# Optimization experiments

Measured on AMD Instinct MI355X. Metric: run time of the kernel, lower is better.

Reference implementation:

```python
import jax, jax.numpy as jnp
import numpy as np

B, N, E = 8, 2048, 2048  # requires N == E (see bmm(value, attn^T) constraint)

def setup_inputs() -> dict:
    key = jax.random.key(0)
    k1, k2, k3 = jax.random.split(key, 3)
    inputs = jax.random.normal(k1, (B, N, E), dtype=jnp.float32)
    # nn.Linear(embed_size, embed_size): weight [E,E], bias [E]
    W = jax.random.normal(k2, (E, E), dtype=jnp.float32) * (1.0 / np.sqrt(E))
    b = jax.random.normal(k3, (E,), dtype=jnp.float32) * 0.01
    gamma = jnp.zeros((), dtype=jnp.float32)  # nn.Parameter(torch.tensor(0.0))
    return {"inputs": inputs, "W": W, "b": b, "gamma": gamma}

def reference(inputs, W, b, gamma):
    # query = Linear(inputs); key = value = inputs
    query = jnp.einsum('bne,fe->bnf', inputs, W) + b          # [B,N,E]
    # scores = bmm(query, key^T) + gamma  -> [B,N,N]
    scores = jnp.einsum('bne,bme->bnm', query, inputs) + gamma
    # softmax over dim=1 (rows, NOT the usual last dim)
    attn = jax.nn.softmax(scores, axis=1)                      # [B,N,N]
    # output = bmm(value, attn^T): out[b,n,m] = sum_e value[b,n,e]*attn[b,m,e]
    out = jnp.einsum('bne,bme->bnm', inputs, attn)             # [B,N,N]
    return out
```

## Files before the change

### kernel.cpp

```cpp
#include <hip/hip_runtime.h>
#include <stdint.h>


typedef _Float16 f16;
typedef f16 f16x8 __attribute__((ext_vector_type(8)));
typedef f16 f16x4 __attribute__((ext_vector_type(4)));
typedef float f32x4 __attribute__((ext_vector_type(4)));

#define ND 2048
#define NNL 4194304L
#define NT 32

static __device__ __forceinline__ void stage16(const void* g, void* l) {
  __builtin_amdgcn_global_load_lds(
      (const __attribute__((address_space(1))) uint32_t*)g,
      (__attribute__((address_space(3))) uint32_t*)l, 16, 0, 0);
}

__global__ void cvt_f16(const float* __restrict__ x, f16* __restrict__ h, int n4) {
  int i = blockIdx.x * 256 + threadIdx.x;
  if (i >= n4) return;
  float4 v = reinterpret_cast<const float4*>(x)[i];
  f16x4 o;
  o.x = (f16)v.x; o.y = (f16)v.y; o.z = (f16)v.z; o.w = (f16)v.w;
  reinterpret_cast<f16x4*>(h)[i] = o;
}

#define RB(d_, o_, kh_) ((((d_) << 2) | ((o_) << 1) | (kh_)) * 16384)

#define STG(gp_, ro_, t_, kh_)                                           \
  do {                                                                   \
    stage16((gp_) + (long)(t_) * 128 + (kh_) * 64, smem + (ro_) + ld0);  \
    stage16((gp_) + 524288L + (long)(t_) * 128 + (kh_) * 64,             \
            smem + (ro_) + ld1);                                         \
  } while (0)

#define FENCE asm volatile("" ::: "memory")

#define PHASE(d_, mh_, kh_, RDB_, STAGE_, WAIT_)                              \
  do {                                                                        \
    const char* ra_ = smem + RB(d_, 0, kh_) + (mh_) * 4096 + aoff;            \
    f16x8 af[4];                                                              \
    af[0] = *(const f16x8*)(ra_);                                             \
    af[1] = *(const f16x8*)(ra_ + 1024);                                      \
    af[2] = *(const f16x8*)(ra_ + 2048);                                      \
    af[3] = *(const f16x8*)(ra_ + 3072);                                      \
    if (RDB_) {                                                               \
      const char* rb_ = smem + RB(d_, 1, kh_) + boff;                         \
      bf[0] = *(const f16x8*)(rb_);                                           \
      bf[1] = *(const f16x8*)(rb_ + 1024);                                    \
      bf[2] = *(const f16x8*)(rb_ + 2048);                                    \
      bf[3] = *(const f16x8*)(rb_ + 3072);                                    \
    }                                                                         \
    STAGE_                                                                    \
    FENCE;                                                                    \
    __builtin_amdgcn_s_barrier();                                             \
    FENCE;                                                                    \
    __builtin_amdgcn_s_setprio(1);                                            \
    _Pragma("unroll") for (int mt_ = 0; mt_ < 4; ++mt_) {                     \
      _Pragma("unroll") for (int nt_ = 0; nt_ < 4; ++nt_) {                   \
        acc[(mh_) * 4 + mt_][nt_] = __builtin_amdgcn_mfma_f32_16x16x32_f16(   \
            af[mt_], bf[nt_], acc[(mh_) * 4 + mt_][nt_], 0, 0, 0);            \
      }                                                                       \
    }                                                                         \
    __builtin_amdgcn_s_setprio(0);                                            \
    WAIT_                                                                     \
    FENCE;                                                                    \
    __builtin_amdgcn_s_barrier();                                             \
    FENCE;                                                                    \
  } while (0)

template <int MODE>
__launch_bounds__(512, 2) __global__
void gemm256(const f16* __restrict__ A, long sA, const f16* __restrict__ B, long sB,
             const float* __restrict__ bias, const float* __restrict__ gamma,
             float* __restrict__ Cf, f16* __restrict__ Ch) {
  __shared__ char smem[131072];

  const int bz = blockIdx.z;
  const long tm = (long)blockIdx.y * 256;
  const long tn = (long)blockIdx.x * 256;
  const int tid = threadIdx.x;
  const int lane = tid & 63;
  const int wid = tid >> 6;
  const int wm = (wid >> 2) << 7;
  const int wn = (wid & 3) << 6;

  const int sg = (tid & 3) ^ ((tid >> 3) & 3);
  const char* gA = (const char*)(A + bz * sA + tm * ND) + (long)(tid >> 2) * 4096 + sg * 16;
  const char* gB = (const char*)(B + bz * sB + tn * ND) + (long)(tid >> 2) * 4096 + sg * 16;
  const uint32_t ld0 = tid * 16u;
  const uint32_t ld1 = 8192u + tid * 16u;

  const int segsw = (((lane >> 4) ^ ((lane >> 1) & 3)) << 4);
  const int lrow = lane & 15;
  const int aoff = (wm + lrow) * 64 + segsw;
  const int boff = (wn + lrow) * 64 + segsw;

  f32x4 acc[8][4] = {};
  f16x8 bf[4];

  STG(gA, RB(0, 0, 0), 0, 0);
  STG(gB, RB(0, 1, 0), 0, 0);
  STG(gA, RB(0, 0, 1), 0, 1);
  STG(gB, RB(0, 1, 1), 0, 1);
  STG(gA, RB(1, 0, 0), 1, 0);
  STG(gB, RB(1, 1, 0), 1, 0);
  asm volatile("s_waitcnt vmcnt(4)" ::: "memory");
  __builtin_amdgcn_s_barrier();
  FENCE;

#pragma unroll 2
  for (int t = 0; t < NT; ++t) {
    const int d = t & 1;
    const int e = d ^ 1;
    PHASE(d, 0, 0, 1, if (t + 1 < NT) STG(gA, RB(e, 0, 1), t + 1, 1);, ;);
    PHASE(d, 1, 0, 0, if (t + 1 < NT) STG(gB, RB(e, 1, 1), t + 1, 1);, ;);
    PHASE(d, 0, 1, 1, if (t + 2 < NT) STG(gA, RB(d, 0, 0), t + 2, 0);, ;);
    PHASE(d, 1, 1, 0, if (t + 2 < NT) STG(gB, RB(d, 1, 0), t + 2, 0);,
          if (t + 2 < NT) { asm volatile("s_waitcnt vmcnt(4)" ::: "memory"); }
          else            { asm volatile("s_waitcnt vmcnt(0)" ::: "memory"); });
  }

  const int rr = (lane >> 4) << 2;
  const int cc = lane & 15;
  const long cb = (long)bz * NNL;
  if constexpr (MODE == 1) {
#pragma unroll
    for (int nt = 0; nt < 4; ++nt) {
      const long col = tn + wn + nt * 16 + cc;
      const float bj = bias[col];
#pragma unroll
      for (int mt = 0; mt < 8; ++mt) {
#pragma unroll
        for (int r = 0; r < 4; ++r) {
          const long row = tm + wm + mt * 16 + rr + r;
          Ch[cb + row * ND + col] = (f16)(acc[mt][nt][r] + bj);
        }
      }
    }
  } else {
    const float g = gamma ? gamma[0] : 0.0f;
#pragma unroll
    for (int mt = 0; mt < 8; ++mt) {
#pragma unroll
      for (int nt = 0; nt < 4; ++nt) {
#pragma unroll
        for (int r = 0; r < 4; ++r) {
          const long row = tm + wm + mt * 16 + rr + r;
          const long col = tn + wn + nt * 16 + cc;
          Cf[cb + row * ND + col] = acc[mt][nt][r] + g;
        }
      }
    }
  }
}

__global__ void stats_partial(const float* __restrict__ S, float* __restrict__ Mp,
                              float* __restrict__ Sp) {
  const int col = blockIdx.x * 256 + threadIdx.x;
  const int seg = blockIdx.y;
  const int b = blockIdx.z;
  const float* p = S + (long)b * NNL + (long)seg * 256 * ND + col;
  float m = -3.4e38f, s = 0.f;
  for (int n = 0; n < 256; ++n) {
    float x = p[(long)n * ND];
    float nm = fmaxf(m, x);
    s = s * __expf(m - nm) + __expf(x - nm);
    m = nm;
  }
  const long o = ((long)b * 8 + seg) * ND + col;
  Mp[o] = m;
  Sp[o] = s;
}

__global__ void stats_combine(const float* __restrict__ Mp, const float* __restrict__ Sp,
                              float* __restrict__ Mx, float* __restrict__ Rs) {
  const int col = blockIdx.x * 256 + threadIdx.x;
  const int b = blockIdx.y;
  float m = -3.4e38f, s = 0.f;
  for (int k = 0; k < 8; ++k) {
    const long o = ((long)b * 8 + k) * ND + col;
    float mk = Mp[o], sk = Sp[o];
    float nm = fmaxf(m, mk);
    s = s * __expf(m - nm) + sk * __expf(mk - nm);
    m = nm;
  }
  Mx[(long)b * ND + col] = m;
  Rs[(long)b * ND + col] = 1.0f / s;
}

__global__ void scale_exp_kernel(const float* __restrict__ S, const float* __restrict__ Mx,
                                 const float* __restrict__ Rs, f16* __restrict__ A) {
  const long i4 = (long)blockIdx.x * 256 + threadIdx.x;
  const long i = i4 * 4;
  const int b = (int)(i >> 22);
  const int col = (int)(i & 2047);
  float4 s = reinterpret_cast<const float4*>(S)[i4];
  float4 m4 = *reinterpret_cast<const float4*>(&Mx[(long)b * ND + col]);
  float4 r4 = *reinterpret_cast<const float4*>(&Rs[(long)b * ND + col]);
  f16x4 o;
  o.x = (f16)(__expf(s.x - m4.x) * r4.x);
  o.y = (f16)(__expf(s.y - m4.y) * r4.y);
  o.z = (f16)(__expf(s.z - m4.z) * r4.z);
  o.w = (f16)(__expf(s.w - m4.w) * r4.w);
  reinterpret_cast<f16x4*>(A)[i4] = o;
}

extern "C" void kernel_launch(void* const* d_in, const int* in_sizes, int n_in,
                              void* d_out, int out_size, void* d_ws, size_t ws_size,
                              hipStream_t stream) {
  (void)in_sizes; (void)n_in; (void)out_size;
  const float* X = (const float*)d_in[0];
  const float* W = (const float*)d_in[1];
  const float* bias = (const float*)d_in[2];
  const float* gamma = (const float*)d_in[3];

  char* ws = (char*)d_ws;
  f16* Xh = (f16*)(ws);
  f16* Wh = (f16*)(ws + 67108864L);
  f16* Qh = (f16*)(ws + 75497472L);
  float* S = (float*)(ws + 142606336L);
  float* Mp = (float*)(ws + 276824064L);
  float* Sp = (float*)(ws + 277348352L);
  float* Mx = (float*)(ws + 277872640L);
  float* Rs = (float*)(ws + 277938176L);
  f16* Amat = Qh;
  if (ws_size < 278003712UL) return;

  cvt_f16<<<32768, 256, 0, stream>>>(X, Xh, 8388608);
  cvt_f16<<<4096, 256, 0, stream>>>(W, Wh, 1048576);

  dim3 gg(8, 8, 8), bb(512);
  gemm256<1><<<gg, bb, 0, stream>>>(Xh, NNL, Wh, 0L, bias, nullptr, nullptr, Qh);
  gemm256<0><<<gg, bb, 0, stream>>>(Qh, NNL, Xh, NNL, nullptr, gamma, S, nullptr);
  stats_partial<<<dim3(8, 8, 8), 256, 0, stream>>>(S, Mp, Sp);
  stats_combine<<<dim3(8, 8), 256, 0, stream>>>(Mp, Sp, Mx, Rs);
  scale_exp_kernel<<<32768, 256, 0, stream>>>(S, Mx, Rs, Amat);
  gemm256<0><<<gg, bb, 0, stream>>>(Xh, NNL, Amat, NNL, nullptr, nullptr,
                                    (float*)d_out, nullptr);
}
```

Baseline: 700.2 us.

## Cut GEMM main-loop barriers from eight to two per k-tile

Removes the barriers before and after each MFMA phase. Instead there is one combined vmcnt/lgkmcnt wait plus barrier after each pair of phases, so the async global->LDS loads run further ahead (vmcnt 8 instead of 4). The last two k-iterations are peeled so the per-stage bounds checks go away. This cuts barrier stalls and lets waves drift apart, but the LDS buffer reuse now depends on a more delicate ordering between stages and reads.

```diff
diff --git a/kernel.cpp b/kernel.cpp
--- a/kernel.cpp
+++ b/kernel.cpp
@@ -37,7 +37,14 @@
 
 #define FENCE asm volatile("" ::: "memory")
 
-#define PHASE(d_, mh_, kh_, RDB_, STAGE_, WAIT_)                              \
+#define SYNC(vm_)                                                        \
+  do {                                                                   \
+    asm volatile("s_waitcnt vmcnt(" #vm_ ") lgkmcnt(0)" ::: "memory");   \
+    __builtin_amdgcn_s_barrier();                                        \
+    FENCE;                                                               \
+  } while (0)
+
+#define PHASE(d_, mh_, kh_, RDB_, STAGE_)                                     \
   do {                                                                        \
     const char* ra_ = smem + RB(d_, 0, kh_) + (mh_) * 4096 + aoff;            \
     f16x8 af[4];                                                              \
@@ -53,9 +60,6 @@
       bf[3] = *(const f16x8*)(rb_ + 3072);                                    \
     }                                                                         \
     STAGE_                                                                    \
-    FENCE;                                                                    \
-    __builtin_amdgcn_s_barrier();                                             \
-    FENCE;                                                                    \
     __builtin_amdgcn_s_setprio(1);                                            \
     _Pragma("unroll") for (int mt_ = 0; mt_ < 4; ++mt_) {                     \
       _Pragma("unroll") for (int nt_ = 0; nt_ < 4; ++nt_) {                   \
@@ -64,10 +68,6 @@
       }                                                                       \
     }                                                                         \
     __builtin_amdgcn_s_setprio(0);                                            \
-    WAIT_                                                                     \
-    FENCE;                                                                    \
-    __builtin_amdgcn_s_barrier();                                             \
-    FENCE;                                                                    \
   } while (0)
 
 template <int MODE>
@@ -106,20 +106,35 @@
   STG(gB, RB(0, 1, 1), 0, 1);
   STG(gA, RB(1, 0, 0), 1, 0);
   STG(gB, RB(1, 1, 0), 1, 0);
-  asm volatile("s_waitcnt vmcnt(4)" ::: "memory");
+  asm volatile("s_waitcnt vmcnt(8)" ::: "memory");
   __builtin_amdgcn_s_barrier();
   FENCE;
 
 #pragma unroll 2
-  for (int t = 0; t < NT; ++t) {
+  for (int t = 0; t < NT - 2; ++t) {
     const int d = t & 1;
     const int e = d ^ 1;
-    PHASE(d, 0, 0, 1, if (t + 1 < NT) STG(gA, RB(e, 0, 1), t + 1, 1);, ;);
-    PHASE(d, 1, 0, 0, if (t + 1 < NT) STG(gB, RB(e, 1, 1), t + 1, 1);, ;);
-    PHASE(d, 0, 1, 1, if (t + 2 < NT) STG(gA, RB(d, 0, 0), t + 2, 0);, ;);
-    PHASE(d, 1, 1, 0, if (t + 2 < NT) STG(gB, RB(d, 1, 0), t + 2, 0);,
-          if (t + 2 < NT) { asm volatile("s_waitcnt vmcnt(4)" ::: "memory"); }
-          else            { asm volatile("s_waitcnt vmcnt(0)" ::: "memory"); });
+    PHASE(d, 0, 0, 1, STG(gA, RB(e, 0, 1), t + 1, 1););
+    PHASE(d, 1, 0, 0, STG(gB, RB(e, 1, 1), t + 1, 1););
+    SYNC(8);
+    PHASE(d, 0, 1, 1, STG(gA, RB(d, 0, 0), t + 2, 0););
+    PHASE(d, 1, 1, 0, STG(gB, RB(d, 1, 0), t + 2, 0););
+    SYNC(8);
+  }
+  {
+    PHASE(0, 0, 0, 1, STG(gA, RB(1, 0, 1), NT - 1, 1););
+    PHASE(0, 1, 0, 0, STG(gB, RB(1, 1, 1), NT - 1, 1););
+    SYNC(8);
+    PHASE(0, 0, 1, 1, ;);
+    PHASE(0, 1, 1, 0, ;);
+    SYNC(4);
+  }
+  {
+    PHASE(1, 0, 0, 1, ;);
+    PHASE(1, 1, 0, 0, ;);
+    SYNC(0);
+    PHASE(1, 0, 1, 1, ;);
+    PHASE(1, 1, 1, 0, ;);
   }
 
   const int rr = (lane >> 4) << 2;
```

New measurement: 692.9 us. No clear change (-1.0%).
